# Optimization experiments

Measured on AMD Instinct MI355X. Metric: run time of the kernel, lower is better.

The kernel has to match this reference:

```python
import jax, jax.numpy as jnp
import numpy as np

B, D, T = 16, 128, 2048      # batch, latent dim, timesteps
NQ, CS = 8, 1024             # num_quantizers, codebook_size


def setup_inputs() -> dict:
    key = jax.random.key(0)
    k1, k2 = jax.random.split(key)
    x = jax.random.normal(k1, (B, D, T), dtype=jnp.float32)
    codebooks = jax.random.normal(k2, (NQ, CS, D), dtype=jnp.float32)
    return {"x": x, "codebooks": codebooks}


def _nearest_codes(xt, cb):
    # xt: [B, T, D]; cb: [C, D] -> quantized [B, T, D] via nearest-neighbor search
    d = (jnp.sum(xt * xt, axis=-1, keepdims=True)
         - 2.0 * jnp.einsum('btd,cd->btc', xt, cb)
         + jnp.sum(cb * cb, axis=-1))          # [B, T, C]
    idx = jnp.argmin(d, axis=-1)               # [B, T]
    return cb[idx]                             # [B, T, D]


def reference(x, codebooks):
    # x: [B, D, T] (channel_last=False); codebooks: [NQ, CS, D]
    nq = codebooks.shape[0]
    q_sum = jnp.zeros_like(x)
    loss_sum = jnp.zeros((x.shape[0],), dtype=x.dtype)
    for i in range(nq):  # fixed small quantizer loop (structurally sequential)
        xt = jnp.transpose(x, (0, 2, 1))                       # [B, T, D]
        q = jnp.transpose(_nearest_codes(xt, codebooks[i]), (0, 2, 1))  # [B, D, T]
        # straight-through estimator (as in lucidrains VectorQuantize)
        q_st = x + jax.lax.stop_gradient(q - x)
        diff = jax.lax.stop_gradient(q_st) - x                 # quantized.detach() - x
        loss = jnp.mean(jnp.reshape(diff * diff, (x.shape[0], -1)), axis=-1)
        q_sum = q_sum + q_st
        loss_sum = loss_sum + loss
        x = x - q_st                                           # residual
    return q_sum, loss_sum
```

## Files before the change

### kernel.cpp

```cpp
#include <hip/hip_runtime.h>

constexpr int Bb  = 16;
constexpr int Dd  = 128;
constexpr int Tt  = 2048;
constexpr int NQn = 8;
constexpr int CSc = 1024;

constexpr int TB   = 128;
constexpr int NCHQ = 16;
constexpr int CHH  = 8192;

typedef _Float16 half8 __attribute__((ext_vector_type(8)));
typedef __attribute__((ext_vector_type(4)))  float f32x4;
typedef __attribute__((ext_vector_type(16))) float f32x16;

__device__ inline void fsplit(float xv, _Float16& h, _Float16& m) {
    _Float16 hh = (__builtin_fabsf(xv) < 6.103515625e-05f) ? (_Float16)0.0f
                                                           : (_Float16)xv;
    float e = xv - (float)hh;
    h = hh;
    m = (_Float16)(e * 4096.0f);
}
__device__ inline float frec(_Float16 h, _Float16 m) {
    return fmaf((float)m, 2.44140625e-4f, (float)h);
}

__device__ inline void gload_lds16(const _Float16* g, _Float16* l) {
    __builtin_amdgcn_global_load_lds(
        (const __attribute__((address_space(1))) void*)g,
        (__attribute__((address_space(3))) void*)l, 16, 0, 0);
}

#define MFMAH(A, B, C) __builtin_amdgcn_mfma_f32_32x32x16_f16(A, B, C, 0, 0, 0)

__global__ __launch_bounds__(64) void split_kernel(const float* __restrict__ cb,
                                                   _Float16* __restrict__ cbS,
                                                   float* __restrict__ cn) {
    const int c     = blockIdx.x * 64 + threadIdx.x;
    const int chunk = c >> 5;
    const int c31   = c & 31;
    const float* p  = cb + (size_t)c * Dd;
    const size_t base = (size_t)chunk * CHH;

    float s0 = 0.f, s1 = 0.f, s2 = 0.f, s3 = 0.f;
#pragma unroll
    for (int ks = 0; ks < 8; ++ks) {
#pragma unroll
        for (int hi2 = 0; hi2 < 2; ++hi2) {
            const int lanew = hi2 * 32 + c31;
            half8 h8, m8;
#pragma unroll
            for (int jj = 0; jj < 8; jj += 4) {
                float4 v = *(const float4*)(p + ks * 16 + hi2 * 8 + jj);
                s0 = fmaf(v.x, v.x, s0);
                s1 = fmaf(v.y, v.y, s1);
                s2 = fmaf(v.z, v.z, s2);
                s3 = fmaf(v.w, v.w, s3);
                _Float16 hh, mm;
                fsplit(v.x, hh, mm); h8[jj + 0] = hh; m8[jj + 0] = mm;
                fsplit(v.y, hh, mm); h8[jj + 1] = hh; m8[jj + 1] = mm;
                fsplit(v.z, hh, mm); h8[jj + 2] = hh; m8[jj + 2] = mm;
                fsplit(v.w, hh, mm); h8[jj + 3] = hh; m8[jj + 3] = mm;
            }
            *(half8*)&cbS[base + (size_t)((0 * 8 + ks) * 64 + lanew) * 8] = h8;
            *(half8*)&cbS[base + (size_t)((8 + ks) * 64 + lanew) * 8]     = m8;
        }
    }
    cn[c] = (s0 + s1) + (s2 + s3);
}

__global__ __launch_bounds__(512) void rvq_mfma(const float* __restrict__ x,
                                                const float* __restrict__ cb,
                                                const _Float16* __restrict__ cbS,
                                                const float* __restrict__ cn_g,
                                                float* __restrict__ out,
                                                float* __restrict__ part) {
    __shared__ __align__(16) _Float16 sA[3][2][CHH];
    __shared__ __align__(16) float    cn_lds[CSc];
    __shared__ float s_best[8][32];
    __shared__ int   s_idx[8][32];
    __shared__ float s_red[4];

    const int tid  = threadIdx.x;
    const int lane = tid & 63;
    const int w    = __builtin_amdgcn_readfirstlane(tid >> 6);
    const int tt   = w >> 1;
    const int h    = w & 1;
    const int l31  = lane & 31;
    const int hi   = lane >> 5;

    const int t0  = blockIdx.x * TB;
    const int b   = t0 >> 11;
    const int tb0 = t0 & (Tt - 1);
    const int tg  = tb0 + tt * 32 + l31;
    const size_t xbase = (size_t)b * Dd * Tt;

    half8 Bh[8], Bm[8];
    float rn;
    {
        float p0 = 0.f, p1 = 0.f, p2 = 0.f, p3 = 0.f;
#pragma unroll
        for (int ks = 0; ks < 8; ++ks) {
            half8 h8, m8;
#pragma unroll
            for (int j = 0; j < 8; ++j) {
                float v = x[xbase + (size_t)(ks * 16 + hi * 8 + j) * Tt + tg];
                _Float16 hh, mm;
                fsplit(v, hh, mm);
                h8[j] = hh; m8[j] = mm;
                if ((j & 3) == 0)      p0 = fmaf(v, v, p0);
                else if ((j & 3) == 1) p1 = fmaf(v, v, p1);
                else if ((j & 3) == 2) p2 = fmaf(v, v, p2);
                else                   p3 = fmaf(v, v, p3);
            }
            Bh[ks] = h8; Bm[ks] = m8;
        }
        float rnp = (p0 + p1) + (p2 + p3);
        rnp += __shfl_xor(rnp, 32, 64);
        rn = rnp;
    }

    float loss_acc = 0.f;

#pragma unroll 1
    for (int q = 0; q < NQn; ++q) {
        *(float2*)&cn_lds[tid * 2] = *(const float2*)&cn_g[(size_t)q * CSc + tid * 2];

        auto STAGE = [&](int ct, int bb) {
            const int gc = q * 32 + h * 16 + ct;
            const _Float16* g = cbS + (size_t)gc * CHH + tt * 2048 + lane * 8;
            _Float16* dl = &sA[bb][h][tt * 2048];
#pragma unroll
            for (int i = 0; i < 4; ++i) gload_lds16(g + i * 512, dl + i * 512);
        };

        STAGE(0, 0);
        STAGE(1, 1);
        asm volatile("s_waitcnt vmcnt(4) lgkmcnt(0)" ::: "memory");
        __builtin_amdgcn_s_barrier();
        asm volatile("" ::: "memory");

        float best = 3.4e38f;
        int   bidx = 0;
        int   buf  = 0;

#pragma unroll 1
        for (int ct = 0; ct < NCHQ; ++ct) {
            const bool iss = (ct + 2) < NCHQ;
            if (iss) {
                int b2 = buf - 1; if (b2 < 0) b2 = 2;
                STAGE(ct + 2, b2);
            }

            const _Float16* ab = &sA[buf][h][0];
            half8 Ah[8], Am[8];
#pragma unroll
            for (int ks = 0; ks < 8; ++ks) {
                Ah[ks] = *(const half8*)&ab[(size_t)((0 * 8 + ks) * 64 + lane) * 8];
                Am[ks] = *(const half8*)&ab[(size_t)((8 + ks) * 64 + lane) * 8];
            }

            f32x16 accA  = {0.f,0.f,0.f,0.f,0.f,0.f,0.f,0.f,0.f,0.f,0.f,0.f,0.f,0.f,0.f,0.f};
            f32x16 accB1 = accA, accB2 = accA;
            __builtin_amdgcn_s_setprio(1);
#pragma unroll
            for (int ks = 0; ks < 8; ++ks) {
                accA  = MFMAH(Ah[ks], Bh[ks], accA);
                accB1 = MFMAH(Ah[ks], Bm[ks], accB1);
                accB2 = MFMAH(Am[ks], Bh[ks], accB2);
            }
            __builtin_amdgcn_s_setprio(0);

            const int cq = h * 512 + ct * 32;
#pragma unroll
            for (int blk = 0; blk < 4; ++blk) {
                f32x4 cn4 = *(const f32x4*)&cn_lds[cq + blk * 8 + hi * 4];
#pragma unroll
                for (int e = 0; e < 4; ++e) {
                    const int i = blk * 4 + e;
                    float dotv = fmaf(accB1[i] + accB2[i], 2.44140625e-4f, accA[i]);
                    float dd = fmaf(-2.f, dotv, rn + cn4[e]);
                    int cid = cq + blk * 8 + hi * 4 + e;
                    if (dd < best) { best = dd; bidx = cid; }
                }
            }

            if (iss) asm volatile("s_waitcnt vmcnt(4)" ::: "memory");
            else     asm volatile("s_waitcnt vmcnt(0)" ::: "memory");
            __builtin_amdgcn_s_barrier();
            asm volatile("" ::: "memory");

            ++buf; if (buf == 3) buf = 0;
        }

        {
            float ob = __shfl_xor(best, 32, 64);
            int   oi = __shfl_xor(bidx, 32, 64);
            if (ob < best || (ob == best && oi < bidx)) { best = ob; bidx = oi; }
        }
        if (hi == 0) { s_best[w][l31] = best; s_idx[w][l31] = bidx; }
        __syncthreads();
        {
            float ob = s_best[w ^ 1][l31];
            int   oi = s_idx[w ^ 1][l31];
            if (ob < best || (ob == best && oi < bidx)) { best = ob; bidx = oi; }
        }
        const int g = bidx;

        {
            const float* cp = cb + ((size_t)q * CSc + g) * Dd + hi * 8;
            float q0 = 0.f, q1 = 0.f, q2 = 0.f, q3 = 0.f;
#pragma unroll
            for (int ks = 0; ks < 8; ++ks) {
                f32x4 ca  = *(const f32x4*)(cp + ks * 16);
                f32x4 cb4 = *(const f32x4*)(cp + ks * 16 + 4);
                half8 h8 = Bh[ks], m8 = Bm[ks];
                half8 nh, nm;
#pragma unroll
                for (int j = 0; j < 8; ++j) {
                    float cj = (j < 4) ? ca[j] : cb4[j - 4];
                    float nv = frec(h8[j], m8[j]) - cj;
                    if ((j & 3) == 0)      q0 = fmaf(nv, nv, q0);
                    else if ((j & 3) == 1) q1 = fmaf(nv, nv, q1);
                    else if ((j & 3) == 2) q2 = fmaf(nv, nv, q2);
                    else                   q3 = fmaf(nv, nv, q3);
                    _Float16 hh, mm;
                    fsplit(nv, hh, mm);
                    nh[j] = hh; nm[j] = mm;
                }
                Bh[ks] = nh; Bm[ks] = nm;
            }
            float rnn = (q0 + q1) + (q2 + q3);
            rnn += __shfl_xor(rnn, 32, 64);
            rn = rnn;
            if (h == 0) loss_acc += rnn;
        }
    }

    if (h == 0) {
#pragma unroll
        for (int ks = 0; ks < 8; ++ks) {
            half8 h8 = Bh[ks], m8 = Bm[ks];
#pragma unroll
            for (int j = 0; j < 8; ++j) {
                size_t off = xbase + (size_t)(ks * 16 + hi * 8 + j) * Tt + tg;
                out[off] = x[off] - frec(h8[j], m8[j]);
            }
        }
        float ls = loss_acc;
#pragma unroll
        for (int off = 32; off > 0; off >>= 1) ls += __shfl_down(ls, off, 64);
        if (lane == 0) s_red[tt] = ls;
    }
    __syncthreads();
    if (tid == 0)
        part[blockIdx.x] = 0.5f * ((s_red[0] + s_red[1]) + (s_red[2] + s_red[3]));
}

__global__ __launch_bounds__(64) void loss_kernel(const float* __restrict__ part,
                                                  float* __restrict__ out_loss) {
    int b = threadIdx.x;
    if (b < Bb) {
        float s = 0.f;
        const int ppb = Tt / TB;
        for (int k = 0; k < ppb; ++k) s += part[b * ppb + k];
        out_loss[b] = s * (1.0f / ((float)Dd * (float)Tt));
    }
}

extern "C" void kernel_launch(void* const* d_in, const int* in_sizes, int n_in,
                              void* d_out, int out_size, void* d_ws, size_t ws_size,
                              hipStream_t stream) {
    const float* x  = (const float*)d_in[0];
    const float* cb = (const float*)d_in[1];
    float* out = (float*)d_out;

    float*    cn   = (float*)d_ws;
    float*    part = cn + NQn * CSc;
    _Float16* cbS  = (_Float16*)(part + 256);

    split_kernel<<<(NQn * CSc) / 64, 64, 0, stream>>>(cb, cbS, cn);

    const int nblocks = (Bb * Tt) / TB;
    rvq_mfma<<<nblocks, 512, 0, stream>>>(x, cb, cbS, cn, out, part);

    loss_kernel<<<1, 64, 0, stream>>>(part, out + (size_t)Bb * Dd * Tt);
}
```

Baseline: 281.6 us.

## Software-pipeline codebook MFMA with deferred argmin evaluation over four LDS buffers

```diff
diff --git a/kernel.cpp b/kernel.cpp
--- a/kernel.cpp
+++ b/kernel.cpp
@@ -75,7 +75,7 @@
                                                 const float* __restrict__ cn_g,
                                                 float* __restrict__ out,
                                                 float* __restrict__ part) {
-    __shared__ __align__(16) _Float16 sA[3][2][CHH];
+    __shared__ __align__(16) _Float16 sA[4][2][CHH];
     __shared__ __align__(16) float    cn_lds[CSc];
     __shared__ float s_best[8][32];
     __shared__ int   s_idx[8][32];
@@ -124,7 +124,11 @@
 
 #pragma unroll 1
     for (int q = 0; q < NQn; ++q) {
-        *(float2*)&cn_lds[tid * 2] = *(const float2*)&cn_g[(size_t)q * CSc + tid * 2];
+        {
+            float2 c2 = *(const float2*)&cn_g[(size_t)q * CSc + tid * 2];
+            c2.x *= 0.5f; c2.y *= 0.5f;
+            *(float2*)&cn_lds[tid * 2] = c2;
+        }
 
         auto STAGE = [&](int ct, int bb) {
             const int gc = q * 32 + h * 16 + ct;
@@ -142,56 +146,67 @@
 
         float best = 3.4e38f;
         int   bidx = 0;
-        int   buf  = 0;
+        f32x16 aA0, aB0, aA1, aB1;
+
+#define DO_MFMA(E, AA, AB)                                                     \
+        {                                                                      \
+            const _Float16* ab = &sA[(E) & 3][h][0];                           \
+            AA = (f32x16){0.f,0.f,0.f,0.f,0.f,0.f,0.f,0.f,                     \
+                          0.f,0.f,0.f,0.f,0.f,0.f,0.f,0.f};                    \
+            AB = AA;                                                           \
+            __builtin_amdgcn_s_setprio(1);                                     \
+            _Pragma("unroll")                                                  \
+            for (int ks = 0; ks < 8; ++ks) {                                   \
+                half8 Ah = *(const half8*)&ab[(size_t)((ks)*64 + lane) * 8];   \
+                half8 Am = *(const half8*)&ab[(size_t)((8+ks)*64 + lane) * 8]; \
+                AA = MFMAH(Ah, Bh[ks], AA);              \
+                AB = MFMAH(Ah, Bm[ks], AB);              \
+                AB = MFMAH(Am, Bh[ks], AB);              \
+            }                                                                  \
+            __builtin_amdgcn_s_setprio(0);                                     \
+        }
+
+#define DO_EVAL(E, AA, AB)                                                     \
+        {                                                                      \
+            const int cq = h * 512 + (E) * 32;                                 \
+            _Pragma("unroll")                                                  \
+            for (int blk = 0; blk < 4; ++blk) {                                \
+                f32x4 ch4 = *(const f32x4*)&cn_lds[cq + blk * 8 + hi * 4];     \
+                _Pragma("unroll")                                              \
+                for (int e2 = 0; e2 < 4; ++e2) {                               \
+                    const int i = blk * 4 + e2;                                \
+                    float dotv = fmaf(AB[i], 2.44140625e-4f, AA[i]);           \
+                    float s = ch4[e2] - dotv;          \
+                    int cid = cq + blk * 8 + hi * 4 + e2;                      \
+                    if (s < best) { best = s; bidx = cid; }      \
+                }                                                              \
+            }                                                                  \
+        }
 
 #pragma unroll 1
-        for (int ct = 0; ct < NCHQ; ++ct) {
-            const bool iss = (ct + 2) < NCHQ;
-            if (iss) {
-                int b2 = buf - 1; if (b2 < 0) b2 = 2;
-                STAGE(ct + 2, b2);
-            }
-
-            const _Float16* ab = &sA[buf][h][0];
-            half8 Ah[8], Am[8];
-#pragma unroll
-            for (int ks = 0; ks < 8; ++ks) {
-                Ah[ks] = *(const half8*)&ab[(size_t)((0 * 8 + ks) * 64 + lane) * 8];
-                Am[ks] = *(const half8*)&ab[(size_t)((8 + ks) * 64 + lane) * 8];
-            }
-
-            f32x16 accA  = {0.f,0.f,0.f,0.f,0.f,0.f,0.f,0.f,0.f,0.f,0.f,0.f,0.f,0.f,0.f,0.f};
-            f32x16 accB1 = accA, accB2 = accA;
-            __builtin_amdgcn_s_setprio(1);
-#pragma unroll
-            for (int ks = 0; ks < 8; ++ks) {
-                accA  = MFMAH(Ah[ks], Bh[ks], accA);
-                accB1 = MFMAH(Ah[ks], Bm[ks], accB1);
-                accB2 = MFMAH(Am[ks], Bh[ks], accB2);
-            }
-            __builtin_amdgcn_s_setprio(0);
-
-            const int cq = h * 512 + ct * 32;
-#pragma unroll
-            for (int blk = 0; blk < 4; ++blk) {
-                f32x4 cn4 = *(const f32x4*)&cn_lds[cq + blk * 8 + hi * 4];
-#pragma unroll
-                for (int e = 0; e < 4; ++e) {
-                    const int i = blk * 4 + e;
-                    float dotv = fmaf(accB1[i] + accB2[i], 2.44140625e-4f, accA[i]);
-                    float dd = fmaf(-2.f, dotv, rn + cn4[e]);
-                    int cid = cq + blk * 8 + hi * 4 + e;
-                    if (dd < best) { best = dd; bidx = cid; }
-                }
-            }
-
-            if (iss) asm volatile("s_waitcnt vmcnt(4)" ::: "memory");
-            else     asm volatile("s_waitcnt vmcnt(0)" ::: "memory");
+        for (int it = 0; it < 8; ++it) {
+            const int e0 = 2 * it, e1 = 2 * it + 1;
+
+            if (it < 7) STAGE(e0 + 2, (e0 + 2) & 3);
+            DO_MFMA(e0, aA0, aB0);
+            if (it > 0) DO_EVAL(e0 - 1, aA1, aB1);
+            if (it < 7) asm volatile("s_waitcnt vmcnt(4)" ::: "memory");
+            else        asm volatile("s_waitcnt vmcnt(0)" ::: "memory");
             __builtin_amdgcn_s_barrier();
             asm volatile("" ::: "memory");
 
-            ++buf; if (buf == 3) buf = 0;
-        }
+            if (it < 7) STAGE(e1 + 2, (e1 + 2) & 3);
+            DO_MFMA(e1, aA1, aB1);
+            DO_EVAL(e0, aA0, aB0);
+            if (it < 7) asm volatile("s_waitcnt vmcnt(4)" ::: "memory");
+            else        asm volatile("s_waitcnt vmcnt(0)" ::: "memory");
+            __builtin_amdgcn_s_barrier();
+            asm volatile("" ::: "memory");
+        }
+        DO_EVAL(15, aA1, aB1);
+
+#undef DO_MFMA
+#undef DO_EVAL
 
         {
             float ob = __shfl_xor(best, 32, 64);
```

New measurement: 291.3 us. +3.5%, slower.
